# Performance work log

Hardware: AMD Instinct MI355X
Metric: run time of the kernel (lower is better)

Reference implementation:

```python
import jax, jax.numpy as jnp
import numpy as np

INPUT_DIM = 1024
K_DIM = 1024
V_DIM = 1024
HEAD = 16
N = 4096


def setup_inputs() -> dict:
    key = jax.random.key(0)
    ks = jax.random.split(key, 6)
    # kaiming_uniform_(a=1): bound = sqrt(6 / ((1+1)*fan_in)) = sqrt(3/fan_in)
    def ku(k, shape):
        fan_in = shape[1]
        b = np.sqrt(3.0 / fan_in)
        return jax.random.uniform(k, shape, jnp.float32, -b, b)
    x = jax.random.normal(ks[0], (1, N, INPUT_DIM), jnp.float32)
    Wq = ku(ks[1], (K_DIM, INPUT_DIM))
    Wk = ku(ks[2], (K_DIM, INPUT_DIM))
    Wv = ku(ks[3], (V_DIM, INPUT_DIM))
    Wo = ku(ks[4], (V_DIM, V_DIM))
    bo = jnp.zeros((V_DIM,), jnp.float32)
    return {"x": x, "Wq": Wq, "Wk": Wk, "Wv": Wv, "Wo": Wo, "bo": bo}


def reference(x, Wq, Wk, Wv, Wo, bo):
    # x: [1, N, C]
    n = x.shape[1]
    hd_k = K_DIM // HEAD
    hd_v = V_DIM // HEAD
    q = jnp.einsum('bnc,kc->bnk', x, Wq).reshape(1, n, HEAD, hd_k).transpose(0, 2, 1, 3)
    k = jnp.einsum('bnc,kc->bnk', x, Wk).reshape(1, n, HEAD, hd_k).transpose(0, 2, 1, 3)
    v = jnp.einsum('bnc,kc->bnk', x, Wv).reshape(1, n, HEAD, hd_v).transpose(0, 2, 1, 3)
    scale = 1.0 / np.sqrt(hd_k).astype(np.float32)
    scores = jnp.einsum('bhqd,bhkd->bhqk', q, k) * scale  # [1,H,N,N]
    attn = jax.nn.softmax(scores, axis=-1)
    ctx = jnp.einsum('bhqk,bhkd->bhqd', attn, v)  # [1,H,N,hd_v]
    ctx = ctx.transpose(0, 2, 1, 3).reshape(1, n, V_DIM)
    out = jnp.einsum('bnv,ov->bno', ctx, Wo) + bo
    return out
```

## Files before the change

kernel.cpp:

```cpp
#include <hip/hip_runtime.h>

typedef short bf16x8 __attribute__((ext_vector_type(8)));
typedef float f32x4 __attribute__((ext_vector_type(4)));
typedef float f32x16 __attribute__((ext_vector_type(16)));
typedef unsigned short u16;
typedef unsigned short u16x8 __attribute__((ext_vector_type(8)));
typedef unsigned int u32;
typedef unsigned int u32x2 __attribute__((ext_vector_type(2)));
typedef unsigned int u32x4 __attribute__((ext_vector_type(4)));

#define MFMA16(a, b, c) __builtin_amdgcn_mfma_f32_16x16x32_bf16((a), (b), (c), 0, 0, 0)
#define MFMA32(a, b, c) __builtin_amdgcn_mfma_f32_32x32x16_bf16((a), (b), (c), 0, 0, 0)

__device__ __forceinline__ u16 f2bf(float f) {
  unsigned u = __builtin_bit_cast(unsigned, f);
  return (u16)((u + 0x7fffu + ((u >> 16) & 1u)) >> 16);
}

__device__ __forceinline__ unsigned cvt_pk_bf16(float lo, float hi) {
  unsigned r;
  asm("v_cvt_pk_bf16_f32 %0, %1, %2" : "=v"(r) : "v"(lo), "v"(hi));
  return r;
}

__device__ __forceinline__ void gload_lds16(const u16* g, u16* lds) {
  __builtin_amdgcn_global_load_lds((__attribute__((address_space(1))) void*)g,
                                   (__attribute__((address_space(3))) void*)lds,
                                   16, 0, 0);
}

__device__ __forceinline__ void publish_barrier() {
  asm volatile("s_waitcnt lgkmcnt(0)" ::: "memory");
  __builtin_amdgcn_sched_barrier(0);
  __builtin_amdgcn_s_barrier();
}

__global__ __launch_bounds__(256) void cvt_all(
    const float* __restrict__ x, const float* __restrict__ w0,
    const float* __restrict__ w1, const float* __restrict__ w2,
    const float* __restrict__ w3, u16* __restrict__ xb, u16* __restrict__ wb) {
  long i = (long)(blockIdx.x * 256 + threadIdx.x) * 8;
  const float* src; u16* dst; long off;
  if (i < 4194304) { src = x; dst = xb; off = i; }
  else {
    long k = i - 4194304; int w = (int)(k >> 20); off = k & 1048575;
    src = (w == 0) ? w0 : (w == 1) ? w1 : (w == 2) ? w2 : w3;
    dst = wb + (long)w * 1048576;
  }
  float4 a = *(const float4*)(src + off);
  float4 b = *(const float4*)(src + off + 4);
  u16x8 o;
  o[0] = f2bf(a.x); o[1] = f2bf(a.y); o[2] = f2bf(a.z); o[3] = f2bf(a.w);
  o[4] = f2bf(b.x); o[5] = f2bf(b.y); o[6] = f2bf(b.z); o[7] = f2bf(b.w);
  *(u16x8*)(dst + off) = o;
}

template <int MODE>
__global__ __launch_bounds__(256) void gemm_bt(
    const u16* __restrict__ A, const u16* __restrict__ Bw,
    u16* __restrict__ Co, float* __restrict__ Cf, const float* __restrict__ bias) {
  constexpr int K = 1024;
  __shared__ u16 As[128 * 32];
  __shared__ u16 Bs[128 * 32];
  const int tid = threadIdx.x, w = tid >> 6, l = tid & 63;
  const int lg = l >> 4, lr = l & 15;
  const int mb = blockIdx.x;
  int mat, nb;
  if (MODE == 0) { mat = blockIdx.y >> 3; nb = blockIdx.y & 7; }
  else           { mat = 0;               nb = blockIdx.y;     }
  const u16* __restrict__ Bp = Bw + (long)mat * 1048576;
  const int wr = w >> 1, wc = w & 1;
  f32x4 acc[4][4] = {};
  const int srow = (l >> 2), scol = (l & 3) * 8;
  for (int kt = 0; kt < K / 32; ++kt) {
    const int kb = kt * 32;
    __syncthreads();
#pragma unroll
    for (int i = 0; i < 2; ++i) {
      int r = w * 32 + i * 16 + srow;
      gload_lds16(A  + (long)(mb * 128 + r) * K + kb + scol, &As[(w * 2 + i) * 512]);
      gload_lds16(Bp + (long)(nb * 128 + r) * K + kb + scol, &Bs[(w * 2 + i) * 512]);
    }
    __syncthreads();
    bf16x8 af[4], bf[4];
#pragma unroll
    for (int m = 0; m < 4; ++m) af[m] = *(const bf16x8*)&As[(wr * 64 + m * 16 + lr) * 32 + lg * 8];
#pragma unroll
    for (int n = 0; n < 4; ++n) bf[n] = *(const bf16x8*)&Bs[(wc * 64 + n * 16 + lr) * 32 + lg * 8];
#pragma unroll
    for (int m = 0; m < 4; ++m)
#pragma unroll
      for (int n = 0; n < 4; ++n)
        acc[m][n] = MFMA16(af[m], bf[n], acc[m][n]);
  }
  const int row0 = mb * 128 + wr * 64, col0 = nb * 128 + wc * 64;
#pragma unroll
  for (int m = 0; m < 4; ++m)
#pragma unroll
    for (int n = 0; n < 4; ++n)
#pragma unroll
      for (int rr = 0; rr < 4; ++rr) {
        int row = row0 + m * 16 + lg * 4 + rr;
        int col = col0 + n * 16 + lr;
        float v = acc[m][n][rr];
        if (MODE == 0) {
          if (mat == 0) v *= 0.18033688011112042f;
          Co[(long)mat * 4194304 + (long)row * 1024 + col] = f2bf(v);
        } else {
          Cf[(long)row * 1024 + col] = v + bias[col];
        }
      }
}

__global__ __launch_bounds__(256) void attn(
    const u16* __restrict__ Qg, const u16* __restrict__ Kg,
    const u16* __restrict__ Vg, u16* __restrict__ Og) {
  __shared__ u16 Ksb[2 * 4096];
  __shared__ u16 Vst[2 * 4160];
  const int tid = threadIdx.x, w = tid >> 6, l = tid & 63;
  const int l31 = l & 31, hi = l >> 5;

  const int lin = blockIdx.x;
  const int xcd = lin & 7, idx = lin >> 3;
  const int head = xcd * 2 + (idx >> 5), qt = idx & 31;
  const int hb = head * 64;
  const int q0 = qt * 128 + w * 32;

  const u16* __restrict__ Kh = Kg + hb;

  bf16x8 qf[4];
#pragma unroll
  for (int st = 0; st < 4; ++st)
    qf[st] = *(const bf16x8*)&Qg[(long)(q0 + l31) * 1024 + hb + st * 16 + hi * 8];

  f32x16 o0 = {}, o1 = {};
  f32x4 lsv = {};

  const int krow = tid >> 3;
  const int ksrc = (((tid & 7) * 16) ^ ((krow & 7) << 4)) >> 1;
  u16* kdst = Ksb + w * 512;

#define KSTAGE(t_, db_)                                                       \
  {                                                                           \
    gload_lds16(Kh + (long)((t_) * 64 + krow) * 1024 + ksrc,                  \
                kdst + (db_) * 4096);                                         \
    gload_lds16(Kh + (long)((t_) * 64 + 32 + krow) * 1024 + ksrc,             \
                kdst + (db_) * 4096 + 2048);                                  \
  }

#define KFRAG(kf_, db_)                                                       \
  {                                                                           \
    _Pragma("unroll") for (int tt = 0; tt < 2; ++tt)                          \
      _Pragma("unroll") for (int st = 0; st < 4; ++st) {                      \
        const int row_ = tt * 32 + l31;                                       \
        const int boff_ = (st * 32 + hi * 16) ^ ((row_ & 7) << 4);            \
        (kf_)[tt][st] =                                                       \
            *(const bf16x8*)&Ksb[(db_) * 4096 + row_ * 64 + (boff_ >> 1)];    \
      }                                                                       \
  }

#define QKT(S0_, S1_, db_)                                                    \
  {                                                                           \
    bf16x8 kf_[2][4];                                                         \
    KFRAG(kf_, db_);                                                          \
    S0_ = (f32x16){};                                                         \
    S1_ = (f32x16){};                                                         \
    __builtin_amdgcn_s_setprio(1);                                            \
    _Pragma("unroll") for (int st = 0; st < 4; ++st) {                        \
      S0_ = MFMA32(kf_[0][st], qf[st], S0_);                                  \
      S1_ = MFMA32(kf_[1][st], qf[st], S1_);                                  \
    }                                                                         \
    __builtin_amdgcn_s_setprio(0);                                            \
  }

#define PACKCHUNK(SX, base_, pb_)                                             \
  {                                                                           \
    u32 a0_ = cvt_pk_bf16((SX)[(base_) + 0], (SX)[(base_) + 1]);              \
    u32 b0_ = cvt_pk_bf16((SX)[(base_) + 4], (SX)[(base_) + 5]);              \
    u32 a1_ = cvt_pk_bf16((SX)[(base_) + 2], (SX)[(base_) + 3]);              \
    u32 b1_ = cvt_pk_bf16((SX)[(base_) + 6], (SX)[(base_) + 7]);              \
    u32x2 r0_ = __builtin_amdgcn_permlane32_swap(a0_, b0_, false, false);     \
    u32x2 r1_ = __builtin_amdgcn_permlane32_swap(a1_, b1_, false, false);     \
    u32x4 fv_;                                                                \
    fv_[0] = r0_[0]; fv_[1] = r1_[0]; fv_[2] = r0_[1]; fv_[3] = r1_[1];       \
    (pb_) = __builtin_bit_cast(bf16x8, fv_);                                  \
  }

  const int vsk = (w & 1) * 32 + (l >> 1);
  const int vsd0 = (w >> 1) * 16 + (l & 1) * 8;
  const int vdbase = (w >> 1) * 1040 + (w & 1) * 512;

#define VSTAGE_TR(t_, db_)                                                    \
  {                                                                           \
    gload_lds16(Vg + (long)((t_) * 64 + vsk) * 1024 + hb + vsd0,              \
                Vst + (db_) * 4160 + vdbase);                                 \
    gload_lds16(Vg + (long)((t_) * 64 + vsk) * 1024 + hb + vsd0 + 32,         \
                Vst + (db_) * 4160 + vdbase + 2080);                          \
  }

  const u32 vtr_base =
      (u32)(unsigned long long)(void*)Vst +
      (u32)((l31 >> 4) * 2080 + (l & 15) * 8 + hi * 256);

#define TRREAD(r_, va_, IMM)                                                  \
  asm volatile("ds_read_b64_tr_b16 %0, %1 offset:" #IMM                       \
               : "=v"(r_) : "v"(va_));

#define FINISH_TR(SC0, SC1, db_)                                              \
  {                                                                           \
    _Pragma("unroll") for (int r = 0; r < 16; ++r) {                          \
      SC0[r] = __builtin_amdgcn_exp2f(SC0[r]);                                \
      SC1[r] = __builtin_amdgcn_exp2f(SC1[r]);                                \
    }                                                                         \
    const u32 va_ = vtr_base + (u32)((db_) * 8320);                           \
    u32x2 t00, t01, t02, t03, t10, t11, t12, t13;                             \
    u32x2 t20, t21, t22, t23, t30, t31, t32, t33;                             \
    TRREAD(t00, va_, 0);    TRREAD(t01, va_, 128);                            \
    TRREAD(t02, va_, 4160); TRREAD(t03, va_, 4288);                           \
    TRREAD(t10, va_, 512);  TRREAD(t11, va_, 640);                            \
    TRREAD(t12, va_, 4672); TRREAD(t13, va_, 4800);                           \
    TRREAD(t20, va_, 1024); TRREAD(t21, va_, 1152);                           \
    TRREAD(t22, va_, 5184); TRREAD(t23, va_, 5312);                           \
    TRREAD(t30, va_, 1536); TRREAD(t31, va_, 1664);                           \
    TRREAD(t32, va_, 5696); TRREAD(t33, va_, 5824);                           \
    bf16x8 pb0, pb1, pb2, pb3;                                                \
    PACKCHUNK(SC0, 0, pb0);                                                   \
    PACKCHUNK(SC0, 8, pb1);                                                   \
    PACKCHUNK(SC1, 0, pb2);                                                   \
    PACKCHUNK(SC1, 8, pb3);                                                   \
    asm volatile("s_waitcnt lgkmcnt(0)" ::: "memory");                        \
    __builtin_amdgcn_sched_barrier(0);     \
    __builtin_amdgcn_s_setprio(1);                                            \
    { u32x4 f_; f_[0]=t00[0]; f_[1]=t00[1]; f_[2]=t01[0]; f_[3]=t01[1];       \
      o0 = MFMA32(__builtin_bit_cast(bf16x8, f_), pb0, o0); }                 \
    { u32x4 f_; f_[0]=t02[0]; f_[1]=t02[1]; f_[2]=t03[0]; f_[3]=t03[1];       \
      o1 = MFMA32(__builtin_bit_cast(bf16x8, f_), pb0, o1); }                 \
    { u32x4 f_; f_[0]=t10[0]; f_[1]=t10[1]; f_[2]=t11[0]; f_[3]=t11[1];       \
      o0 = MFMA32(__builtin_bit_cast(bf16x8, f_), pb1, o0); }                 \
    { u32x4 f_; f_[0]=t12[0]; f_[1]=t12[1]; f_[2]=t13[0]; f_[3]=t13[1];       \
      o1 = MFMA32(__builtin_bit_cast(bf16x8, f_), pb1, o1); }                 \
    { u32x4 f_; f_[0]=t20[0]; f_[1]=t20[1]; f_[2]=t21[0]; f_[3]=t21[1];       \
      o0 = MFMA32(__builtin_bit_cast(bf16x8, f_), pb2, o0); }                 \
    { u32x4 f_; f_[0]=t22[0]; f_[1]=t22[1]; f_[2]=t23[0]; f_[3]=t23[1];       \
      o1 = MFMA32(__builtin_bit_cast(bf16x8, f_), pb2, o1); }                 \
    { u32x4 f_; f_[0]=t30[0]; f_[1]=t30[1]; f_[2]=t31[0]; f_[3]=t31[1];       \
      o0 = MFMA32(__builtin_bit_cast(bf16x8, f_), pb3, o0); }                 \
    { u32x4 f_; f_[0]=t32[0]; f_[1]=t32[1]; f_[2]=t33[0]; f_[3]=t33[1];       \
      o1 = MFMA32(__builtin_bit_cast(bf16x8, f_), pb3, o1); }                 \
    __builtin_amdgcn_s_setprio(0);                                            \
    _Pragma("unroll") for (int r2 = 0; r2 < 4; ++r2)                          \
      _Pragma("unroll") for (int j = 0; j < 4; ++j)                           \
        lsv[j] += SC0[r2 * 4 + j] + SC1[r2 * 4 + j];                          \
  }

  f32x16 Sa0, Sa1, Sb0, Sb1;

  KSTAGE(0, 0);
  VSTAGE_TR(0, 0);
  asm volatile("s_waitcnt vmcnt(0)" ::: "memory");
  publish_barrier();
  QKT(Sa0, Sa1, 0);
  KSTAGE(1, 1);
  asm volatile("s_waitcnt vmcnt(0)" ::: "memory");
  publish_barrier();

#define BODY_TR(t_, db_, SC0, SC1, SN0, SN1, kst_)                            \
  {                                                                           \
    if (kst_) KSTAGE((t_) + 2, db_);                                          \
    VSTAGE_TR((t_) + 1, (db_) ^ 1);                                           \
    QKT(SN0, SN1, (db_) ^ 1);                                                 \
    FINISH_TR(SC0, SC1, db_);                                                 \
    asm volatile("s_waitcnt vmcnt(0)" ::: "memory");                          \
    publish_barrier();                                                        \
  }

  for (int i = 0; i < 31; ++i) {
    BODY_TR(2 * i, 0, Sa0, Sa1, Sb0, Sb1, true);
    BODY_TR(2 * i + 1, 1, Sb0, Sb1, Sa0, Sa1, true);
  }
  BODY_TR(62, 0, Sa0, Sa1, Sb0, Sb1, false);
  FINISH_TR(Sb0, Sb1, 1);

  {
    float sls = (lsv[0] + lsv[1]) + (lsv[2] + lsv[3]);
    float s = sls + __shfl_xor(sls, 32);
    float inv = 1.0f / s;
#pragma unroll
    for (int dt = 0; dt < 2; ++dt) {
#pragma unroll
      for (int r2 = 0; r2 < 4; ++r2) {
        float v0 = dt ? o1[r2 * 4 + 0] : o0[r2 * 4 + 0];
        float v1 = dt ? o1[r2 * 4 + 1] : o0[r2 * 4 + 1];
        float v2 = dt ? o1[r2 * 4 + 2] : o0[r2 * 4 + 2];
        float v3 = dt ? o1[r2 * 4 + 3] : o0[r2 * 4 + 3];
        uint2 pk;
        pk.x = cvt_pk_bf16(v0 * inv, v1 * inv);
        pk.y = cvt_pk_bf16(v2 * inv, v3 * inv);
        const int d0 = dt * 32 + 8 * r2 + 4 * hi;
        *(uint2*)&Og[(long)(q0 + l31) * 1024 + hb + d0] = pk;
      }
    }
  }
#undef KSTAGE
#undef KFRAG
#undef QKT
#undef PACKCHUNK
#undef VSTAGE_TR
#undef TRREAD
#undef FINISH_TR
#undef BODY_TR
}

extern "C" void kernel_launch(void* const* d_in, const int* in_sizes, int n_in,
                              void* d_out, int out_size, void* d_ws, size_t ws_size,
                              hipStream_t stream) {
  const float* x  = (const float*)d_in[0];
  const float* Wq = (const float*)d_in[1];
  const float* Wk = (const float*)d_in[2];
  const float* Wv = (const float*)d_in[3];
  const float* Wo = (const float*)d_in[4];
  const float* bo = (const float*)d_in[5];
  float* out = (float*)d_out;

  u16* xb  = (u16*)d_ws;
  u16* wb  = xb + 4194304;
  u16* qkv = wb + 4194304;
  u16* ctx = qkv + 3 * 4194304;

  cvt_all<<<dim3(4096), dim3(256), 0, stream>>>(x, Wq, Wk, Wv, Wo, xb, wb);
  gemm_bt<0><<<dim3(32, 24), dim3(256), 0, stream>>>(xb, wb, qkv, nullptr, nullptr);
  attn<<<dim3(512), dim3(256), 0, stream>>>(qkv, qkv + 4194304, qkv + 8388608, ctx);
  gemm_bt<1><<<dim3(32, 8), dim3(256), 0, stream>>>(ctx, wb + 3 * 1048576, nullptr, out, bo);
}
```

Before: 159.0 us.

## Use BK=64 XOR-swizzled LDS tiles in GEMMs and smaller output-GEMM tiles

```diff
diff --git a/kernel.cpp b/kernel.cpp
--- a/kernel.cpp
+++ b/kernel.cpp
@@ -55,43 +55,49 @@
   *(u16x8*)(dst + off) = o;
 }
 
-template <int MODE>
-__global__ __launch_bounds__(256) void gemm_bt(
+__global__ __launch_bounds__(256) void gemm_qkv(
     const u16* __restrict__ A, const u16* __restrict__ Bw,
-    u16* __restrict__ Co, float* __restrict__ Cf, const float* __restrict__ bias) {
-  constexpr int K = 1024;
-  __shared__ u16 As[128 * 32];
-  __shared__ u16 Bs[128 * 32];
+    u16* __restrict__ Co) {
+  __shared__ u16 As[128 * 64];
+  __shared__ u16 Bs[128 * 64];
   const int tid = threadIdx.x, w = tid >> 6, l = tid & 63;
   const int lg = l >> 4, lr = l & 15;
   const int mb = blockIdx.x;
-  int mat, nb;
-  if (MODE == 0) { mat = blockIdx.y >> 3; nb = blockIdx.y & 7; }
-  else           { mat = 0;               nb = blockIdx.y;     }
+  const int mat = blockIdx.y >> 3, nb = blockIdx.y & 7;
   const u16* __restrict__ Bp = Bw + (long)mat * 1048576;
   const int wr = w >> 1, wc = w & 1;
   f32x4 acc[4][4] = {};
-  const int srow = (l >> 2), scol = (l & 3) * 8;
-  for (int kt = 0; kt < K / 32; ++kt) {
-    const int kb = kt * 32;
+  const int srow = w * 8 + (l >> 3);
+  const int scol = ((l & 7) * 8) ^ (((l >> 3) & 7) << 3);
+  for (int kt = 0; kt < 16; ++kt) {
+    const int kb = kt * 64;
     __syncthreads();
 #pragma unroll
-    for (int i = 0; i < 2; ++i) {
-      int r = w * 32 + i * 16 + srow;
-      gload_lds16(A  + (long)(mb * 128 + r) * K + kb + scol, &As[(w * 2 + i) * 512]);
-      gload_lds16(Bp + (long)(nb * 128 + r) * K + kb + scol, &Bs[(w * 2 + i) * 512]);
+    for (int call = 0; call < 4; ++call) {
+      int r = call * 32 + srow;
+      gload_lds16(A  + (long)(mb * 128 + r) * 1024 + kb + scol, &As[call * 2048 + w * 512]);
+      gload_lds16(Bp + (long)(nb * 128 + r) * 1024 + kb + scol, &Bs[call * 2048 + w * 512]);
     }
     __syncthreads();
-    bf16x8 af[4], bf[4];
-#pragma unroll
-    for (int m = 0; m < 4; ++m) af[m] = *(const bf16x8*)&As[(wr * 64 + m * 16 + lr) * 32 + lg * 8];
-#pragma unroll
-    for (int n = 0; n < 4; ++n) bf[n] = *(const bf16x8*)&Bs[(wc * 64 + n * 16 + lr) * 32 + lg * 8];
-#pragma unroll
-    for (int m = 0; m < 4; ++m)
-#pragma unroll
-      for (int n = 0; n < 4; ++n)
-        acc[m][n] = MFMA16(af[m], bf[n], acc[m][n]);
+#pragma unroll
+    for (int ksub = 0; ksub < 2; ++ksub) {
+      bf16x8 af[4], bf[4];
+#pragma unroll
+      for (int m = 0; m < 4; ++m) {
+        const int row_ = wr * 64 + m * 16 + lr;
+        af[m] = *(const bf16x8*)&As[row_ * 64 + ((ksub * 32 + lg * 8) ^ ((row_ & 7) << 3))];
+      }
+#pragma unroll
+      for (int n = 0; n < 4; ++n) {
+        const int row_ = wc * 64 + n * 16 + lr;
+        bf[n] = *(const bf16x8*)&Bs[row_ * 64 + ((ksub * 32 + lg * 8) ^ ((row_ & 7) << 3))];
+      }
+#pragma unroll
+      for (int m = 0; m < 4; ++m)
+#pragma unroll
+        for (int n = 0; n < 4; ++n)
+          acc[m][n] = MFMA16(af[m], bf[n], acc[m][n]);
+    }
   }
   const int row0 = mb * 128 + wr * 64, col0 = nb * 128 + wc * 64;
 #pragma unroll
@@ -103,12 +109,67 @@
         int row = row0 + m * 16 + lg * 4 + rr;
         int col = col0 + n * 16 + lr;
         float v = acc[m][n][rr];
-        if (MODE == 0) {
-          if (mat == 0) v *= 0.18033688011112042f;
-          Co[(long)mat * 4194304 + (long)row * 1024 + col] = f2bf(v);
-        } else {
-          Cf[(long)row * 1024 + col] = v + bias[col];
-        }
+        if (mat == 0) v *= 0.18033688011112042f;
+        Co[(long)mat * 4194304 + (long)row * 1024 + col] = f2bf(v);
+      }
+}
+
+__global__ __launch_bounds__(256) void gemm_out(
+    const u16* __restrict__ A, const u16* __restrict__ Bw,
+    float* __restrict__ Cf, const float* __restrict__ bias) {
+  __shared__ u16 As[64 * 64];
+  __shared__ u16 Bs[128 * 64];
+  const int tid = threadIdx.x, w = tid >> 6, l = tid & 63;
+  const int lg = l >> 4, lr = l & 15;
+  const int mb = blockIdx.x, nb = blockIdx.y;
+  const int wr = w >> 1, wc = w & 1;
+  f32x4 acc[2][4] = {};
+  const int srow = w * 8 + (l >> 3);
+  const int scol = ((l & 7) * 8) ^ (((l >> 3) & 7) << 3);
+  for (int kt = 0; kt < 16; ++kt) {
+    const int kb = kt * 64;
+    __syncthreads();
+#pragma unroll
+    for (int call = 0; call < 2; ++call) {
+      int r = call * 32 + srow;
+      gload_lds16(A + (long)(mb * 64 + r) * 1024 + kb + scol, &As[call * 2048 + w * 512]);
+    }
+#pragma unroll
+    for (int call = 0; call < 4; ++call) {
+      int r = call * 32 + srow;
+      gload_lds16(Bw + (long)(nb * 128 + r) * 1024 + kb + scol, &Bs[call * 2048 + w * 512]);
+    }
+    __syncthreads();
+#pragma unroll
+    for (int ksub = 0; ksub < 2; ++ksub) {
+      bf16x8 af[2], bf[4];
+#pragma unroll
+      for (int m = 0; m < 2; ++m) {
+        const int row_ = wr * 32 + m * 16 + lr;
+        af[m] = *(const bf16x8*)&As[row_ * 64 + ((ksub * 32 + lg * 8) ^ ((row_ & 7) << 3))];
+      }
+#pragma unroll
+      for (int n = 0; n < 4; ++n) {
+        const int row_ = wc * 64 + n * 16 + lr;
+        bf[n] = *(const bf16x8*)&Bs[row_ * 64 + ((ksub * 32 + lg * 8) ^ ((row_ & 7) << 3))];
+      }
+#pragma unroll
+      for (int m = 0; m < 2; ++m)
+#pragma unroll
+        for (int n = 0; n < 4; ++n)
+          acc[m][n] = MFMA16(af[m], bf[n], acc[m][n]);
+    }
+  }
+  const int row0 = mb * 64 + wr * 32, col0 = wc * 64;
+#pragma unroll
+  for (int m = 0; m < 2; ++m)
+#pragma unroll
+    for (int n = 0; n < 4; ++n)
+#pragma unroll
+      for (int rr = 0; rr < 4; ++rr) {
+        int row = row0 + m * 16 + lg * 4 + rr;
+        int col = nb * 128 + col0 + n * 16 + lr;
+        Cf[(long)row * 1024 + col] = acc[m][n][rr] + bias[col];
       }
 }
 
@@ -328,7 +389,7 @@
   u16* ctx = qkv + 3 * 4194304;
 
   cvt_all<<<dim3(4096), dim3(256), 0, stream>>>(x, Wq, Wk, Wv, Wo, xb, wb);
-  gemm_bt<0><<<dim3(32, 24), dim3(256), 0, stream>>>(xb, wb, qkv, nullptr, nullptr);
+  gemm_qkv<<<dim3(32, 24), dim3(256), 0, stream>>>(xb, wb, qkv);
   attn<<<dim3(512), dim3(256), 0, stream>>>(qkv, qkv + 4194304, qkv + 8388608, ctx);
-  gemm_bt<1><<<dim3(32, 8), dim3(256), 0, stream>>>(ctx, wb + 3 * 1048576, nullptr, out, bo);
-}
+  gemm_out<<<dim3(64, 8), dim3(256), 0, stream>>>(ctx, wb + 3 * 1048576, out, bo);
+}
```

Result: no change. 159.5 us (+0.3%).
